# Kernel tuning notes

Hardware: AMD Instinct MI355X
Metric: run time of the kernel (lower is better)

The kernel has to match this reference:

```python
import jax, jax.numpy as jnp
import numpy as np

D_MODEL = 512
NUM_HEADS = 8
HEAD_DIM = D_MODEL // NUM_HEADS
NUM_RBF = 16
MAX_DIST = 2.0
SCALE = HEAD_DIM ** -0.5
SIGMA = MAX_DIST / NUM_RBF


def setup_inputs() -> dict:
    key = jax.random.key(0)
    ks = jax.random.split(key, 8)
    B, L = 4, 1024
    x = jax.random.normal(ks[0], (B, L, D_MODEL), dtype=jnp.float32)
    coords = jax.random.normal(ks[1], (B, L, 3), dtype=jnp.float32)
    mask = jnp.ones((B, L), dtype=bool)
    # torch Linear weights stored transposed: (in, out)
    s = 1.0 / np.sqrt(D_MODEL)
    Wqkv = jax.random.uniform(ks[2], (D_MODEL, 3 * D_MODEL), jnp.float32, -s, s)
    bqkv = jax.random.uniform(ks[3], (3 * D_MODEL,), jnp.float32, -s, s)
    sr = 1.0 / np.sqrt(NUM_RBF)
    Wbias = jax.random.uniform(ks[4], (NUM_RBF, NUM_HEADS), jnp.float32, -sr, sr)
    bbias = jax.random.uniform(ks[5], (NUM_HEADS,), jnp.float32, -sr, sr)
    Wout = jax.random.uniform(ks[6], (D_MODEL, D_MODEL), jnp.float32, -s, s)
    bout = jax.random.uniform(ks[7], (D_MODEL,), jnp.float32, -s, s)
    return {"x": x, "coords": coords, "mask": mask,
            "Wqkv": Wqkv, "bqkv": bqkv, "Wbias": Wbias, "bbias": bbias,
            "Wout": Wout, "bout": bout}


def reference(x, coords, mask, Wqkv, bqkv, Wbias, bbias, Wout, bout):
    B, L, _ = x.shape
    qkv = x @ Wqkv + bqkv                              # (B,L,3*d)
    qkv = qkv.reshape(B, L, 3, NUM_HEADS, HEAD_DIM)
    qkv = jnp.transpose(qkv, (2, 0, 3, 1, 4))          # (3,B,H,L,hd)
    q, k, v = qkv[0], qkv[1], qkv[2]
    logits = jnp.einsum('bhqd,bhkd->bhqk', q, k) * SCALE
    # pairwise euclidean distances with safe sqrt (zero grad at d=0)
    diff = coords[:, :, None, :] - coords[:, None, :, :]  # (B,L,L,3)
    d2 = jnp.sum(diff * diff, axis=-1)
    dists = jnp.where(d2 > 0, jnp.sqrt(jnp.where(d2 > 0, d2, 1.0)), 0.0)
    mu = jnp.linspace(0.0, MAX_DIST, NUM_RBF)
    rbf = jnp.exp(-(dists[..., None] - mu) ** 2 / (2.0 * SIGMA ** 2))  # (B,L,L,R)
    geo = rbf @ Wbias + bbias                          # (B,L,L,H)
    logits = logits + jnp.transpose(geo, (0, 3, 1, 2))  # (B,H,L,L)
    neg_inf = jnp.finfo(logits.dtype).min
    logits = jnp.where(mask[:, None, None, :], logits, neg_inf)
    w = jax.nn.softmax(logits, axis=-1)
    out = jnp.einsum('bhqk,bhkd->bhqd', w, v)
    out = jnp.transpose(out, (0, 2, 1, 3)).reshape(B, L, D_MODEL)
    return out @ Wout + bout
```

## Files before the change

### kernel.cpp

```cpp
#include <hip/hip_runtime.h>
#include <hip/hip_bf16.h>

typedef unsigned short u16;
typedef unsigned int   u32;
typedef __attribute__((ext_vector_type(8))) __bf16 bf16x8;
typedef __attribute__((ext_vector_type(8))) unsigned short u16x8;
typedef __attribute__((ext_vector_type(4))) float  f32x4;

#define LOG2E 1.4426950408889634f
#define SC2   (0.125f * LOG2E)
#define NTAB  512
#define INV_DT128 21802.667f

__device__ __forceinline__ u16 f2bf(float f) {
  u32 u = __float_as_uint(f);
  u32 r = (u + 0x7FFFu + ((u >> 16) & 1u)) >> 16;
  return (u16)r;
}

__device__ __forceinline__ void gld16(const void* g, void* l) {
  __builtin_amdgcn_global_load_lds((const __attribute__((address_space(1))) void*)g,
                                   (__attribute__((address_space(3))) void*)l,
                                   16, 0, 0);
}

__device__ __forceinline__ int sigma64(int l) {
  return (l & ~0x3C) | ((l >> 2) & 0x0C) | ((l << 2) & 0x30);
}

__device__ __forceinline__ void tr64_body(const float* __restrict__ in, u16* __restrict__ out,
                                          int R, int C, int c0, int r0, int tid,
                                          float (*tile)[65]) {
  const int cl = tid & 63, rl = tid >> 6;
#pragma unroll
  for (int p = 0; p < 16; ++p) {
    int row = p * 4 + rl;
    tile[row][cl] = in[(size_t)(r0 + row) * C + c0 + cl];
  }
  __syncthreads();
#pragma unroll
  for (int p = 0; p < 16; ++p) {
    int cc = p * 4 + rl;
    out[(size_t)(c0 + cc) * R + r0 + cl] = f2bf(tile[cl][cc]);
  }
}

__global__ __launch_bounds__(256) void prep(
    const float* __restrict__ x, const float* __restrict__ Wqkv, const float* __restrict__ Wout,
    const float* __restrict__ Wbias, const float* __restrict__ bbias,
    const float* __restrict__ coords,
    u16* __restrict__ xb, u16* __restrict__ wqkvT, u16* __restrict__ woutT,
    u32* __restrict__ gpack, u16* __restrict__ didx) {
  __shared__ float tile[64][65];
  const int bx = blockIdx.x, tid = threadIdx.x;
  if (bx < 2048) {
    int i = bx * 256 + tid;
    float4 v = ((const float4*)x)[i];
    ushort4 o;
    o.x = f2bf(v.x); o.y = f2bf(v.y); o.z = f2bf(v.z); o.w = f2bf(v.w);
    ((ushort4*)xb)[i] = o;
  } else if (bx < 2240) {
    int t = bx - 2048;
    tr64_body(Wqkv, wqkvT, 512, 1536, (t % 24) * 64, (t / 24) * 64, tid, tile);
  } else if (bx < 2304) {
    int t = bx - 2240;
    tr64_body(Wout, woutT, 512, 512, (t & 7) * 64, (t >> 3) * 64, tid, tile);
  } else if (bx < 2306) {
    int i = (bx - 2304) * 256 + tid;
    float d0 = (float)i * (3.0f / 511.0f);
    float d1 = (float)(i + 1) * (3.0f / 511.0f);
    float g0[8], g1[8];
#pragma unroll
    for (int h = 0; h < 8; ++h) { g0[h] = bbias[h]; g1[h] = bbias[h]; }
#pragma unroll
    for (int r = 0; r < 16; ++r) {
      float mu = (float)r * (2.0f / 15.0f);
      float e0 = __expf(-(d0 - mu) * (d0 - mu) * 32.0f);
      float e1 = __expf(-(d1 - mu) * (d1 - mu) * 32.0f);
#pragma unroll
      for (int h = 0; h < 8; ++h) {
        g0[h] += e0 * Wbias[r * 8 + h];
        g1[h] += e1 * Wbias[r * 8 + h];
      }
    }
#pragma unroll
    for (int h = 0; h < 8; ++h) {
      u32 lo = f2bf(g0[h] * LOG2E);
      u32 hi = f2bf((g1[h] - g0[h]) * (LOG2E / 128.0f));
      gpack[h * NTAB + i] = (hi << 16) | lo;
    }
  } else {
    __shared__ float rcf[12];
    int bi = bx - 2306;
    int b = bi >> 8, it = bi & 255;
    int i0 = it * 4;
    if (tid < 12) rcf[tid] = coords[(size_t)b * 3072 + i0 * 3 + tid];
    __syncthreads();
#pragma unroll
    for (int jt = 0; jt < 4; ++jt) {
      int j = jt * 256 + tid;
      float cx = coords[((size_t)b * 1024 + j) * 3 + 0];
      float cy = coords[((size_t)b * 1024 + j) * 3 + 1];
      float cz = coords[((size_t)b * 1024 + j) * 3 + 2];
#pragma unroll
      for (int ii = 0; ii < 4; ++ii) {
        float dx = rcf[ii * 3 + 0] - cx, dy = rcf[ii * 3 + 1] - cy, dz = rcf[ii * 3 + 2] - cz;
        float d = sqrtf(fmaf(dx, dx, fmaf(dy, dy, dz * dz)));
        float t = fminf(d * INV_DT128, 65407.0f);
        didx[((size_t)b << 20) + (size_t)(i0 + ii) * 1024 + j] = (u16)(t + 0.5f);
      }
    }
  }
}

template <int EPI, int NT, int MT>
__global__ __launch_bounds__(256) void gemm_bt(
    const u16* __restrict__ A, const u16* __restrict__ Bt, const float* __restrict__ bias,
    float* __restrict__ Cf, u16* __restrict__ Qb, u16* __restrict__ Kb, u16* __restrict__ Vt,
    int N, int K) {
  __shared__ __attribute__((aligned(16))) u16 AsBs[MT * 64 * 64 + NT * 16 * 64];
  u16* As = AsBs;
  u16* Bs = AsBs + MT * 64 * 64;
  const int tid = threadIdx.x;
  const int w = tid >> 6, lane = tid & 63;
  const int lm = lane & 15, lg = lane >> 4;
  const int m0 = blockIdx.y * (MT * 64), n0 = blockIdx.x * (NT * 16);
  const f32x4 z4 = {0.f, 0.f, 0.f, 0.f};
  f32x4 acc[MT][NT];
#pragma unroll
  for (int mt = 0; mt < MT; ++mt)
#pragma unroll
    for (int nt = 0; nt < NT; ++nt) acc[mt][nt] = z4;

  for (int k0 = 0; k0 < K; k0 += 64) {
    __syncthreads();
#pragma unroll
    for (int j = 0; j < 2 * MT; ++j) {
      int cidx = j * 256 + tid;
      int row = cidx >> 3, c8 = cidx & 7;
      gld16(A + (size_t)(m0 + row) * K + k0 + c8 * 8, &As[cidx * 8]);
    }
#pragma unroll
    for (int j = 0; j < NT / 2; ++j) {
      int cidx = j * 256 + tid;
      int row = cidx >> 3, c8 = cidx & 7;
      gld16(Bt + (size_t)(n0 + row) * K + k0 + c8 * 8, &Bs[cidx * 8]);
    }
    __syncthreads();
#pragma unroll
    for (int c = 0; c < 2; ++c) {
      const int ko = c * 32 + lg * 8;
      bf16x8 af[MT], bfr[NT];
#pragma unroll
      for (int mt = 0; mt < MT; ++mt)
        af[mt] = *(const bf16x8*)&As[(w * (MT * 16) + mt * 16 + lm) * 64 + ko];
#pragma unroll
      for (int nt = 0; nt < NT; ++nt)
        bfr[nt] = *(const bf16x8*)&Bs[(nt * 16 + lm) * 64 + ko];
#pragma unroll
      for (int mt = 0; mt < MT; ++mt)
#pragma unroll
        for (int nt = 0; nt < NT; ++nt)
          acc[mt][nt] = __builtin_amdgcn_mfma_f32_16x16x32_bf16(af[mt], bfr[nt], acc[mt][nt], 0, 0, 0);
    }
  }

  if (EPI == 0 && (n0 >> 9) == 2) {
    const int hh = (n0 & 511) >> 6;
    const int bh = (m0 >> 10) * 8 + hh;
    const int l0 = m0 & 1023;
    __syncthreads();
#pragma unroll
    for (int mt = 0; mt < MT; ++mt)
#pragma unroll
      for (int nt = 0; nt < NT; ++nt) {
        const float bv = bias[n0 + nt * 16 + lm];
#pragma unroll
        for (int r = 0; r < 4; ++r) {
          int ml = w * (MT * 16) + mt * 16 + lg * 4 + r;
          int lp = (ml & 64) | sigma64(ml & 63);
          AsBs[(nt * 16 + lm) * 132 + lp] = f2bf(acc[mt][nt][r] + bv);
        }
      }
    __syncthreads();
    const int row = tid >> 2, seg = tid & 3;
    const u16* src = &AsBs[row * 132 + seg * 32];
    uint4 q0 = *(const uint4*)(src);
    uint4 q1 = *(const uint4*)(src + 8);
    uint4 q2 = *(const uint4*)(src + 16);
    uint4 q3 = *(const uint4*)(src + 24);
    u16* dst = Vt + ((size_t)bh * 64 + row) * 1024 + l0 + seg * 32;
    *(uint4*)(dst)      = q0;
    *(uint4*)(dst + 8)  = q1;
    *(uint4*)(dst + 16) = q2;
    *(uint4*)(dst + 24) = q3;
    return;
  }

#pragma unroll
  for (int mt = 0; mt < MT; ++mt) {
#pragma unroll
    for (int nt = 0; nt < NT; ++nt) {
      const int n = n0 + nt * 16 + lm;
      const float bv = bias[n];
#pragma unroll
      for (int r = 0; r < 4; ++r) {
        const int m = m0 + w * (MT * 16) + mt * 16 + lg * 4 + r;
        float v = acc[mt][nt][r] + bv;
        if (EPI == 1) {
          Cf[(size_t)m * N + n] = v;
        } else {
          int b = m >> 10, l = m & 1023;
          int which = n >> 9, f = n & 511, h = f >> 6, o = f & 63;
          u16 hv = f2bf(v);
          int lp = (l & ~63) | sigma64(l & 63);
          if (which == 0)      Qb[(((size_t)(b * 8 + h)) * 1024 + l) * 64 + o] = hv;
          else                 Kb[(((size_t)(b * 8 + h)) * 1024 + lp) * 64 + o] = hv;
        }
      }
    }
  }
}

__global__ __launch_bounds__(512, 4) void attn_kernel(
    const u16* __restrict__ Qb, const u16* __restrict__ Kb, const u16* __restrict__ Vt,
    const u16* __restrict__ didx, const u32* __restrict__ gpack, u16* __restrict__ Ob) {
  __shared__ __attribute__((aligned(16))) char smem[53248];
  u32* tab = (u32*)smem;

  const int tid = threadIdx.x;
  const int w = tid >> 6, lane = tid & 63;
  const int lm = lane & 15, lg = lane >> 4;
  const int half = w >> 2, wq = w & 3;
  const int bid = (blockIdx.x & 7) * 64 + (blockIdx.x >> 3);
  const int qt = bid & 15, bh = bid >> 4, h = bh & 7, b = bh >> 3;

  u16* Ks = (u16*)(smem + 2048 + half * 16384);
  u16* Vs = (u16*)(smem + 10240 + half * 16384);
  u16* Ps = (u16*)(smem + 34816 + w * 2304);

  tab[tid] = gpack[(size_t)h * NTAB + tid];

  const int qrow0 = qt * 64 + wq * 16;
  bf16x8 qf[2];
  {
    const u16* qp = Qb + ((size_t)bh * 1024 + qrow0 + lm) * 64 + lg * 8;
    qf[0] = *(const bf16x8*)(qp);
    qf[1] = *(const bf16x8*)(qp + 32);
  }
  const int kb0 = half * 512;
  const u16* dptr = didx + ((size_t)b << 20) + (size_t)(qrow0 + lm) * 1024 + kb0 + lg * 16;

  float l = 0.f;
  const f32x4 z4 = {0.f, 0.f, 0.f, 0.f};
  f32x4 Oa[4];
#pragma unroll
  for (int ft = 0; ft < 4; ++ft) Oa[ft] = z4;

  const int sw = lm & 7;
  const int htid = tid & 255;

  for (int i = 0; i < 8; ++i) {
    __syncthreads();
#pragma unroll
    for (int j = 0; j < 2; ++j) {
      int cidx = j * 256 + htid;
      int row = cidx >> 3, c8s = (cidx & 7) ^ (row & 7);
      gld16(Kb + ((size_t)bh * 1024 + kb0 + i * 64 + row) * 64 + c8s * 8, Ks + cidx * 8);
      gld16(Vt + ((size_t)bh * 64 + row) * 1024 + kb0 + i * 64 + c8s * 8, Vs + cidx * 8);
    }
    u16x8 dv0 = *(const u16x8*)(dptr + i * 64);
    u16x8 dv1 = *(const u16x8*)(dptr + i * 64 + 8);
    __syncthreads();

    f32x4 S[4];
#pragma unroll
    for (int nt = 0; nt < 4; ++nt) S[nt] = z4;
#pragma unroll
    for (int c = 0; c < 2; ++c) {
#pragma unroll
      for (int nt = 0; nt < 4; ++nt) {
        bf16x8 kf = *(const bf16x8*)&Ks[(nt * 16 + lm) * 64 + (((c * 4 + lg) ^ sw) * 8)];
        S[nt] = __builtin_amdgcn_mfma_f32_16x16x32_bf16(kf, qf[c], S[nt], 0, 0, 0);
      }
    }
    float rs = 0.f;
#pragma unroll
    for (int nt = 0; nt < 4; ++nt)
#pragma unroll
      for (int r = 0; r < 4; ++r) {
        int t = nt * 4 + r;
        u32 u = (t < 8) ? (u32)dv0[t] : (u32)dv1[t - 8];
        u32 pk = tab[u >> 7];
        float fr = (float)(u & 127u);
        float g0 = __uint_as_float(pk << 16);
        float dg = __uint_as_float(pk & 0xffff0000u);
        float p = exp2f(fmaf(S[nt][r], SC2, fmaf(fr, dg, g0)));
        S[nt][r] = p;
        rs += p;
      }
    l += rs;
#pragma unroll
    for (int nt = 0; nt < 4; ++nt) {
      __hip_bfloat162 p01 = __float22bfloat162_rn(make_float2(S[nt][0], S[nt][1]));
      __hip_bfloat162 p23 = __float22bfloat162_rn(make_float2(S[nt][2], S[nt][3]));
      *(uint2*)&Ps[lm * 72 + nt * 16 + lg * 4] = make_uint2(*(u32*)&p01, *(u32*)&p23);
    }
    bf16x8 pa[2];
    pa[0] = *(const bf16x8*)&Ps[lm * 72 + lg * 8];
    pa[1] = *(const bf16x8*)&Ps[lm * 72 + 32 + lg * 8];
#pragma unroll
    for (int ft = 0; ft < 4; ++ft)
#pragma unroll
      for (int c = 0; c < 2; ++c) {
        bf16x8 vf = *(const bf16x8*)&Vs[(ft * 16 + lm) * 64 + (((c * 4 + lg) ^ sw) * 8)];
        Oa[ft] = __builtin_amdgcn_mfma_f32_16x16x32_bf16(pa[c], vf, Oa[ft], 0, 0, 0);
      }
  }

  l += __shfl_xor(l, 16);
  l += __shfl_xor(l, 32);

  __syncthreads();
  float* mO = (float*)(smem + 2048);
  float* mL = (float*)(smem + 18432);
  if (half == 1) {
#pragma unroll
    for (int ft = 0; ft < 4; ++ft)
#pragma unroll
      for (int r = 0; r < 4; ++r)
        mO[wq * 1024 + (lg * 4 + r) * 64 + ft * 16 + lm] = Oa[ft][r];
    if (lg == 0) mL[wq * 16 + lm] = l;
  }
  __syncthreads();
  if (half == 0) {
    l += mL[wq * 16 + lm];
#pragma unroll
    for (int r = 0; r < 4; ++r) {
      float lr = __shfl(l, lg * 4 + r);
      float inv = 1.0f / lr;
      int qrow = qrow0 + lg * 4 + r;
      size_t o = ((size_t)b * 1024 + qrow) * 512 + h * 64;
#pragma unroll
      for (int ft = 0; ft < 4; ++ft) {
        float vsum = Oa[ft][r] + mO[wq * 1024 + (lg * 4 + r) * 64 + ft * 16 + lm];
        Ob[o + ft * 16 + lm] = f2bf(vsum * inv);
      }
    }
  }
}

extern "C" void kernel_launch(void* const* d_in, const int* in_sizes, int n_in,
                              void* d_out, int out_size, void* d_ws, size_t ws_size,
                              hipStream_t stream) {
  const float* x      = (const float*)d_in[0];
  const float* coords = (const float*)d_in[1];
  const float* Wqkv   = (const float*)d_in[3];
  const float* bqkv   = (const float*)d_in[4];
  const float* Wbias  = (const float*)d_in[5];
  const float* bbias  = (const float*)d_in[6];
  const float* Wout   = (const float*)d_in[7];
  const float* bout   = (const float*)d_in[8];
  float* out = (float*)d_out;

  char* ws = (char*)d_ws;
  u16* xb     = (u16*)(ws + 0);
  u16* wqkvT  = (u16*)(ws + 4194304);
  u16* woutT  = (u16*)(ws + 5767168);
  u32* gpack  = (u32*)(ws + 6291456);
  u16* didx   = (u16*)(ws + 8388608);
  u16* qb     = (u16*)(ws + 16777216);
  u16* kb     = (u16*)(ws + 20971520);
  u16* vtb    = (u16*)(ws + 25165824);
  u16* attnb  = (u16*)(ws + 29360128);

  prep<<<3330, 256, 0, stream>>>(x, Wqkv, Wout, Wbias, bbias, coords,
                                 xb, wqkvT, woutT, gpack, didx);
  gemm_bt<0, 4, 2><<<dim3(24, 32), 256, 0, stream>>>(xb, wqkvT, bqkv, nullptr, qb, kb, vtb, 1536, 512);
  attn_kernel<<<512, 512, 0, stream>>>(qb, kb, vtb, didx, gpack, attnb);
  gemm_bt<1, 4, 1><<<dim3(8, 64), 256, 0, stream>>>(attnb, woutT, bout, out, nullptr, nullptr, nullptr, 512, 512);
}
```

Before: 136.6 us.

## Halve attention block size with two query tiles per wave and register prefetch

Attention blocks now use 256 threads, and each wave handles 32 query rows as two 16-row MFMA tiles. This reuses every K/V LDS fragment across twice as many MFMAs. The async global-to-LDS loads are replaced by register-staged prefetch of the next K/V tile and distance indices, overlapping global loads with compute. This raises register pressure and lowers the wave count per block, which may reduce occupancy and latency hiding.

```diff
diff --git a/kernel.cpp b/kernel.cpp
--- a/kernel.cpp
+++ b/kernel.cpp
@@ -222,7 +222,7 @@
   }
 }
 
-__global__ __launch_bounds__(512, 4) void attn_kernel(
+__global__ __launch_bounds__(256, 2) void attn_kernel(
     const u16* __restrict__ Qb, const u16* __restrict__ Kb, const u16* __restrict__ Vt,
     const u16* __restrict__ didx, const u32* __restrict__ gpack, u16* __restrict__ Ob) {
   __shared__ __attribute__((aligned(16))) char smem[53248];
@@ -231,95 +231,132 @@
   const int tid = threadIdx.x;
   const int w = tid >> 6, lane = tid & 63;
   const int lm = lane & 15, lg = lane >> 4;
-  const int half = w >> 2, wq = w & 3;
+  const int half = w >> 1, wq = w & 1;
+  const int ht = tid & 127;
   const int bid = (blockIdx.x & 7) * 64 + (blockIdx.x >> 3);
   const int qt = bid & 15, bh = bid >> 4, h = bh & 7, b = bh >> 3;
 
   u16* Ks = (u16*)(smem + 2048 + half * 16384);
   u16* Vs = (u16*)(smem + 10240 + half * 16384);
-  u16* Ps = (u16*)(smem + 34816 + w * 2304);
+  u16* Ps = (u16*)(smem + 34816 + w * 4608);
 
   tab[tid] = gpack[(size_t)h * NTAB + tid];
-
-  const int qrow0 = qt * 64 + wq * 16;
-  bf16x8 qf[2];
+  tab[256 + tid] = gpack[(size_t)h * NTAB + 256 + tid];
+
+  const int qrow0 = qt * 64 + wq * 32;
+  bf16x8 qf0[2], qf1[2];
   {
     const u16* qp = Qb + ((size_t)bh * 1024 + qrow0 + lm) * 64 + lg * 8;
-    qf[0] = *(const bf16x8*)(qp);
-    qf[1] = *(const bf16x8*)(qp + 32);
+    qf0[0] = *(const bf16x8*)(qp);
+    qf0[1] = *(const bf16x8*)(qp + 32);
+    qf1[0] = *(const bf16x8*)(qp + 16 * 64);
+    qf1[1] = *(const bf16x8*)(qp + 16 * 64 + 32);
   }
   const int kb0 = half * 512;
   const u16* dptr = didx + ((size_t)b << 20) + (size_t)(qrow0 + lm) * 1024 + kb0 + lg * 16;
 
-  float l = 0.f;
+  float l0 = 0.f, l1 = 0.f;
   const f32x4 z4 = {0.f, 0.f, 0.f, 0.f};
-  f32x4 Oa[4];
-#pragma unroll
-  for (int ft = 0; ft < 4; ++ft) Oa[ft] = z4;
+  f32x4 Oa0[4], Oa1[4];
+#pragma unroll
+  for (int ft = 0; ft < 4; ++ft) { Oa0[ft] = z4; Oa1[ft] = z4; }
 
   const int sw = lm & 7;
-  const int htid = tid & 255;
+
+  uint4 kr[4], vr[4];
+  u16x8 dc[4], dn[4];
+#pragma unroll
+  for (int j = 0; j < 4; ++j) {
+    int cidx = j * 128 + ht, row = cidx >> 3, c8 = cidx & 7;
+    kr[j] = *(const uint4*)(Kb + ((size_t)bh * 1024 + kb0 + row) * 64 + c8 * 8);
+    vr[j] = *(const uint4*)(Vt + ((size_t)bh * 64 + row) * 1024 + kb0 + c8 * 8);
+  }
+  dc[0] = *(const u16x8*)(dptr);
+  dc[1] = *(const u16x8*)(dptr + 8);
+  dc[2] = *(const u16x8*)(dptr + 16384);
+  dc[3] = *(const u16x8*)(dptr + 16384 + 8);
 
   for (int i = 0; i < 8; ++i) {
     __syncthreads();
 #pragma unroll
-    for (int j = 0; j < 2; ++j) {
-      int cidx = j * 256 + htid;
-      int row = cidx >> 3, c8s = (cidx & 7) ^ (row & 7);
-      gld16(Kb + ((size_t)bh * 1024 + kb0 + i * 64 + row) * 64 + c8s * 8, Ks + cidx * 8);
-      gld16(Vt + ((size_t)bh * 64 + row) * 1024 + kb0 + i * 64 + c8s * 8, Vs + cidx * 8);
-    }
-    u16x8 dv0 = *(const u16x8*)(dptr + i * 64);
-    u16x8 dv1 = *(const u16x8*)(dptr + i * 64 + 8);
-    __syncthreads();
-
-    f32x4 S[4];
-#pragma unroll
-    for (int nt = 0; nt < 4; ++nt) S[nt] = z4;
+    for (int j = 0; j < 4; ++j) {
+      int cidx = j * 128 + ht, row = cidx >> 3, c8 = cidx & 7;
+      int off = row * 64 + ((c8 ^ (row & 7)) * 8);
+      *(uint4*)&Ks[off] = kr[j];
+      *(uint4*)&Vs[off] = vr[j];
+    }
+    if (i < 7) {
+#pragma unroll
+      for (int j = 0; j < 4; ++j) {
+        int cidx = j * 128 + ht, row = cidx >> 3, c8 = cidx & 7;
+        kr[j] = *(const uint4*)(Kb + ((size_t)bh * 1024 + kb0 + (i + 1) * 64 + row) * 64 + c8 * 8);
+        vr[j] = *(const uint4*)(Vt + ((size_t)bh * 64 + row) * 1024 + kb0 + (i + 1) * 64 + c8 * 8);
+      }
+      dn[0] = *(const u16x8*)(dptr + (i + 1) * 64);
+      dn[1] = *(const u16x8*)(dptr + (i + 1) * 64 + 8);
+      dn[2] = *(const u16x8*)(dptr + 16384 + (i + 1) * 64);
+      dn[3] = *(const u16x8*)(dptr + 16384 + (i + 1) * 64 + 8);
+    }
+    __syncthreads();
+
+    f32x4 S0[4], S1[4];
+#pragma unroll
+    for (int nt = 0; nt < 4; ++nt) { S0[nt] = z4; S1[nt] = z4; }
 #pragma unroll
     for (int c = 0; c < 2; ++c) {
 #pragma unroll
       for (int nt = 0; nt < 4; ++nt) {
         bf16x8 kf = *(const bf16x8*)&Ks[(nt * 16 + lm) * 64 + (((c * 4 + lg) ^ sw) * 8)];
-        S[nt] = __builtin_amdgcn_mfma_f32_16x16x32_bf16(kf, qf[c], S[nt], 0, 0, 0);
-      }
-    }
-    float rs = 0.f;
+        S0[nt] = __builtin_amdgcn_mfma_f32_16x16x32_bf16(kf, qf0[c], S0[nt], 0, 0, 0);
+        S1[nt] = __builtin_amdgcn_mfma_f32_16x16x32_bf16(kf, qf1[c], S1[nt], 0, 0, 0);
+      }
+    }
+    float rs0 = 0.f, rs1 = 0.f;
 #pragma unroll
     for (int nt = 0; nt < 4; ++nt)
 #pragma unroll
       for (int r = 0; r < 4; ++r) {
         int t = nt * 4 + r;
-        u32 u = (t < 8) ? (u32)dv0[t] : (u32)dv1[t - 8];
-        u32 pk = tab[u >> 7];
-        float fr = (float)(u & 127u);
-        float g0 = __uint_as_float(pk << 16);
-        float dg = __uint_as_float(pk & 0xffff0000u);
-        float p = exp2f(fmaf(S[nt][r], SC2, fmaf(fr, dg, g0)));
-        S[nt][r] = p;
-        rs += p;
-      }
-    l += rs;
+        u32 u0 = (t < 8) ? (u32)dc[0][t] : (u32)dc[1][t - 8];
+        u32 u1 = (t < 8) ? (u32)dc[2][t] : (u32)dc[3][t - 8];
+        u32 pk0 = tab[u0 >> 7], pk1 = tab[u1 >> 7];
+        float fr0 = (float)(u0 & 127u), fr1 = (float)(u1 & 127u);
+        float p0 = exp2f(fmaf(S0[nt][r], SC2,
+                    fmaf(fr0, __uint_as_float(pk0 & 0xffff0000u), __uint_as_float(pk0 << 16))));
+        float p1 = exp2f(fmaf(S1[nt][r], SC2,
+                    fmaf(fr1, __uint_as_float(pk1 & 0xffff0000u), __uint_as_float(pk1 << 16))));
+        S0[nt][r] = p0; rs0 += p0;
+        S1[nt][r] = p1; rs1 += p1;
+      }
+    l0 += rs0; l1 += rs1;
 #pragma unroll
     for (int nt = 0; nt < 4; ++nt) {
-      __hip_bfloat162 p01 = __float22bfloat162_rn(make_float2(S[nt][0], S[nt][1]));
-      __hip_bfloat162 p23 = __float22bfloat162_rn(make_float2(S[nt][2], S[nt][3]));
-      *(uint2*)&Ps[lm * 72 + nt * 16 + lg * 4] = make_uint2(*(u32*)&p01, *(u32*)&p23);
-    }
-    bf16x8 pa[2];
-    pa[0] = *(const bf16x8*)&Ps[lm * 72 + lg * 8];
-    pa[1] = *(const bf16x8*)&Ps[lm * 72 + 32 + lg * 8];
+      __hip_bfloat162 a01 = __float22bfloat162_rn(make_float2(S0[nt][0], S0[nt][1]));
+      __hip_bfloat162 a23 = __float22bfloat162_rn(make_float2(S0[nt][2], S0[nt][3]));
+      *(uint2*)&Ps[lm * 72 + nt * 16 + lg * 4] = make_uint2(*(u32*)&a01, *(u32*)&a23);
+      __hip_bfloat162 b01 = __float22bfloat162_rn(make_float2(S1[nt][0], S1[nt][1]));
+      __hip_bfloat162 b23 = __float22bfloat162_rn(make_float2(S1[nt][2], S1[nt][3]));
+      *(uint2*)&Ps[(16 + lm) * 72 + nt * 16 + lg * 4] = make_uint2(*(u32*)&b01, *(u32*)&b23);
+    }
+    bf16x8 pa0[2], pa1[2];
+    pa0[0] = *(const bf16x8*)&Ps[lm * 72 + lg * 8];
+    pa0[1] = *(const bf16x8*)&Ps[lm * 72 + 32 + lg * 8];
+    pa1[0] = *(const bf16x8*)&Ps[(16 + lm) * 72 + lg * 8];
+    pa1[1] = *(const bf16x8*)&Ps[(16 + lm) * 72 + 32 + lg * 8];
 #pragma unroll
     for (int ft = 0; ft < 4; ++ft)
 #pragma unroll
       for (int c = 0; c < 2; ++c) {
         bf16x8 vf = *(const bf16x8*)&Vs[(ft * 16 + lm) * 64 + (((c * 4 + lg) ^ sw) * 8)];
-        Oa[ft] = __builtin_amdgcn_mfma_f32_16x16x32_bf16(pa[c], vf, Oa[ft], 0, 0, 0);
-      }
-  }
-
-  l += __shfl_xor(l, 16);
-  l += __shfl_xor(l, 32);
+        Oa0[ft] = __builtin_amdgcn_mfma_f32_16x16x32_bf16(pa0[c], vf, Oa0[ft], 0, 0, 0);
+        Oa1[ft] = __builtin_amdgcn_mfma_f32_16x16x32_bf16(pa1[c], vf, Oa1[ft], 0, 0, 0);
+      }
+#pragma unroll
+    for (int j = 0; j < 4; ++j) dc[j] = dn[j];
+  }
+
+  l0 += __shfl_xor(l0, 16); l0 += __shfl_xor(l0, 32);
+  l1 += __shfl_xor(l1, 16); l1 += __shfl_xor(l1, 32);
 
   __syncthreads();
   float* mO = (float*)(smem + 2048);
@@ -328,23 +365,30 @@
 #pragma unroll
     for (int ft = 0; ft < 4; ++ft)
 #pragma unroll
-      for (int r = 0; r < 4; ++r)
-        mO[wq * 1024 + (lg * 4 + r) * 64 + ft * 16 + lm] = Oa[ft][r];
-    if (lg == 0) mL[wq * 16 + lm] = l;
+      for (int r = 0; r < 4; ++r) {
+        mO[wq * 2048 + (lg * 4 + r) * 64 + ft * 16 + lm] = Oa0[ft][r];
+        mO[wq * 2048 + (16 + lg * 4 + r) * 64 + ft * 16 + lm] = Oa1[ft][r];
+      }
+    if (lg == 0) { mL[wq * 32 + lm] = l0; mL[wq * 32 + 16 + lm] = l1; }
   }
   __syncthreads();
   if (half == 0) {
-    l += mL[wq * 16 + lm];
+    l0 += mL[wq * 32 + lm];
+    l1 += mL[wq * 32 + 16 + lm];
 #pragma unroll
     for (int r = 0; r < 4; ++r) {
-      float lr = __shfl(l, lg * 4 + r);
-      float inv = 1.0f / lr;
-      int qrow = qrow0 + lg * 4 + r;
-      size_t o = ((size_t)b * 1024 + qrow) * 512 + h * 64;
+      float lr0 = __shfl(l0, lg * 4 + r);
+      float lr1 = __shfl(l1, lg * 4 + r);
+      float inv0 = 1.0f / lr0, inv1 = 1.0f / lr1;
+      int q0r = qrow0 + lg * 4 + r;
+      size_t o0 = ((size_t)b * 1024 + q0r) * 512 + h * 64;
+      size_t o1 = ((size_t)b * 1024 + q0r + 16) * 512 + h * 64;
 #pragma unroll
       for (int ft = 0; ft < 4; ++ft) {
-        float vsum = Oa[ft][r] + mO[wq * 1024 + (lg * 4 + r) * 64 + ft * 16 + lm];
-        Ob[o + ft * 16 + lm] = f2bf(vsum * inv);
+        float v0 = Oa0[ft][r] + mO[wq * 2048 + (lg * 4 + r) * 64 + ft * 16 + lm];
+        float v1 = Oa1[ft][r] + mO[wq * 2048 + (16 + lg * 4 + r) * 64 + ft * 16 + lm];
+        Ob[o0 + ft * 16 + lm] = f2bf(v0 * inv0);
+        Ob[o1 + ft * 16 + lm] = f2bf(v1 * inv1);
       }
     }
   }
@@ -377,6 +421,6 @@
   prep<<<3330, 256, 0, stream>>>(x, Wqkv, Wout, Wbias, bbias, coords,
                                  xb, wqkvT, woutT, gpack, didx);
   gemm_bt<0, 4, 2><<<dim3(24, 32), 256, 0, stream>>>(xb, wqkvT, bqkv, nullptr, qb, kb, vtb, 1536, 512);
-  attn_kernel<<<512, 512, 0, stream>>>(qb, kb, vtb, didx, gpack, attnb);
+  attn_kernel<<<512, 256, 0, stream>>>(qb, kb, vtb, didx, gpack, attnb);
   gemm_bt<1, 4, 1><<<dim3(8, 64), 256, 0, stream>>>(attnb, woutT, bout, out, nullptr, nullptr, nullptr, 512, 512);
 }
```

Result: slower. 162.5 us (+19.0%).
